# Performance work log

Hardware: AMD Instinct MI355X
Metric: run time of the kernel (lower is better)

## Reference

```python
import jax, jax.numpy as jnp
import numpy as np

N_HEADS = 16


def setup_inputs() -> dict:
    key = jax.random.key(0)
    ks = jax.random.split(key, 8)
    B, S, D = 4, 2048, 1024
    scale = 1.0 / np.sqrt(D)
    return {
        "x": jax.random.normal(ks[0], (B, S, D), dtype=jnp.float32),
        "Wq": jax.random.normal(ks[1], (D, D), dtype=jnp.float32) * scale,
        "bq": jax.random.normal(ks[2], (D,), dtype=jnp.float32) * 0.01,
        "Wk": jax.random.normal(ks[3], (D, D), dtype=jnp.float32) * scale,
        "bk": jax.random.normal(ks[4], (D,), dtype=jnp.float32) * 0.01,
        "Wv": jax.random.normal(ks[5], (D, D), dtype=jnp.float32) * scale,
        "bv": jax.random.normal(ks[6], (D,), dtype=jnp.float32) * 0.01,
        "mask": jax.random.randint(ks[7], (B, S), 0, 2, dtype=jnp.int32),
    }


def reference(x, Wq, bq, Wk, bk, Wv, bv, mask):
    B, S, D = x.shape
    H = N_HEADS
    W = D // H
    # QKV projections (Linear with weight stored input-major: y = x @ W + b)
    q = (x @ Wq + bq).reshape(B, S, H, W).transpose(0, 2, 1, 3)  # (B,H,S,W)
    k = (x @ Wk + bk).reshape(B, S, H, W).transpose(0, 2, 1, 3)
    v = (x @ Wv + bv).reshape(B, S, H, W).transpose(0, 2, 1, 3)
    # scaled dot-product scores: (B,H,S,S)
    scores = jnp.einsum("bhsw,bhtw->bhst", q, k) / jnp.sqrt(jnp.asarray(W, x.dtype))
    # mask==1 means masked (subtract large constant), per original code
    scores = scores - 10000.0 * mask[:, None, None, :].astype(x.dtype)
    attn = jax.nn.softmax(scores, axis=-1)  # dropout p=0 -> identity
    h = jnp.einsum("bhst,bhtw->bhsw", attn, v)  # (B,H,S,W)
    h = h.transpose(0, 2, 1, 3).reshape(B, S, D)
    return h
```

## Files before the change

kernel.cpp:

```cpp
#include <hip/hip_runtime.h>
#include <math.h>

#define B_NUM 4
#define S_LEN 2048
#define D_DIM 1024
#define H_NUM 16
#define W_DIM 64

typedef float4 f4;
typedef _Float16 f16;
typedef f16 f16x8 __attribute__((ext_vector_type(8)));
typedef f16 f16x4 __attribute__((ext_vector_type(4)));
typedef float floatx4 __attribute__((ext_vector_type(4)));

#define GLOAD_LDS16(gp, lp)                                                     \
    __builtin_amdgcn_global_load_lds(                                           \
        (const __attribute__((address_space(1))) void*)(gp),                    \
        (__attribute__((address_space(3))) void*)(lp), 16, 0, 0)

#define TR_BLOCKS   768
#define CAST_BLOCKS 8192

__global__ __launch_bounds__(256) void prep_kernel(
    const int* __restrict__ mask, short* __restrict__ fwdmap,
    int* __restrict__ cnt,
    const float* __restrict__ Wq, const float* __restrict__ Wk,
    const float* __restrict__ Wv, f16* __restrict__ wt16,
    const float* __restrict__ x, f16* __restrict__ x16)
{
    __shared__ __align__(16) char smraw[64 * 68 * 4];
    const int bx  = blockIdx.x;
    const int tid = threadIdx.x;

    if (bx < 4) {
        int* sc = (int*)smraw;
        const int b  = bx;
        const int t0 = tid * 8;
#pragma unroll
        for (int j = 0; j < 8; ++j) fwdmap[b * S_LEN + t0 + j] = 0;
        int kept[8], c = 0;
#pragma unroll
        for (int j = 0; j < 8; ++j) {
            kept[j] = (mask[b * S_LEN + t0 + j] == 0);
            c += kept[j];
        }
        sc[tid] = c;
        __syncthreads();
        for (int off = 1; off < 256; off <<= 1) {
            int add = (tid >= off) ? sc[tid - off] : 0;
            __syncthreads();
            sc[tid] += add;
            __syncthreads();
        }
        int base = sc[tid] - c;
#pragma unroll
        for (int j = 0; j < 8; ++j)
            if (kept[j]) fwdmap[b * S_LEN + (base++)] = (short)(t0 + j);
        if (tid == 255) {
            cnt[b * 4 + 0] = sc[255];
            cnt[b * 4 + 1] = (sc[255] + 63) & ~63;
            cnt[b * 4 + 2] = (sc[255] + 127) & ~127;
            cnt[b * 4 + 3] = (sc[255] + 255) & ~255;
        }
    } else if (bx < 4 + TR_BLOCKS) {
        float (*ts)[68] = (float(*)[68])smraw;
        const int idx = bx - 4;
        const int k0 = (idx & 15) * 64;
        const int n0 = ((idx >> 4) & 15) * 64;
        const int z  = idx >> 8;
        const float* Wsel = (z == 0) ? Wq : (z == 1) ? Wk : Wv;
        f16* outp = wt16 + (size_t)z * D_DIM * D_DIM;

        const int r  = tid >> 4;
        const int c4 = (tid & 15) * 4;
#pragma unroll
        for (int i = 0; i < 4; ++i) {
            f4 t = *(const f4*)&Wsel[(size_t)(k0 + r + i * 16) * D_DIM + n0 + c4];
            *(f4*)&ts[r + i * 16][c4] = t;
        }
        __syncthreads();
#pragma unroll
        for (int i = 0; i < 4; ++i) {
            int id2 = tid + i * 256;
            int nl = id2 >> 4;
            int k4 = (id2 & 15) * 4;
            f16x4 o;
#pragma unroll
            for (int j = 0; j < 4; ++j) o[j] = (f16)ts[k4 + j][nl];
            *(f16x4*)&outp[(size_t)(n0 + nl) * D_DIM + k0 + k4] = o;
        }
    } else {
        const size_t i = (size_t)(bx - 4 - TR_BLOCKS) * 256 + tid;
        f4 t = *(const f4*)&x[i * 4];
        f16x4 o;
        o[0] = (f16)t.x; o[1] = (f16)t.y; o[2] = (f16)t.z; o[3] = (f16)t.w;
        *(f16x4*)&x16[i * 4] = o;
    }
}

#define QSTAGE(BUF, K0) do {                                                    \
    _Pragma("unroll") for (int it_ = 0; it_ < 4; ++it_) {                       \
        int chunk_ = wid * 4 + it_;                                             \
        GLOAD_LDS16(&x16[(size_t)arows[it_] * D_DIM + (K0) + scw],              \
                    &As[BUF][chunk_ * 512]);                                    \
        GLOAD_LDS16(&Bg[(size_t)(chunk_ * 8 + srow) * D_DIM + (K0) + scw],      \
                    &Bs[BUF][chunk_ * 512]);                                    \
    } } while (0)

#define QCOMPUTE(BUF) do {                                                      \
    _Pragma("unroll") for (int kh_ = 0; kh_ < 2; ++kh_) {                       \
        const int csw_ = ((kh_ * 4 + quad) ^ (lx & 7)) * 8;                     \
        f16x8 af_[4], bf_[4];                                                   \
        _Pragma("unroll") for (int tm_ = 0; tm_ < 4; ++tm_)                     \
            af_[tm_] = *(const f16x8*)&As[BUF][(wm * 64 + tm_ * 16 + lx) * 64 + csw_]; \
        _Pragma("unroll") for (int tn_ = 0; tn_ < 4; ++tn_)                     \
            bf_[tn_] = *(const f16x8*)&Bs[BUF][(wn * 64 + tn_ * 16 + lx) * 64 + csw_]; \
        _Pragma("unroll") for (int tm_ = 0; tm_ < 4; ++tm_)                     \
        _Pragma("unroll") for (int tn_ = 0; tn_ < 4; ++tn_)                     \
            acc[tm_][tn_] = __builtin_amdgcn_mfma_f32_16x16x32_f16(             \
                af_[tm_], bf_[tn_], acc[tm_][tn_], 0, 0, 0);                    \
    } } while (0)

#define QVM0BAR() do {                                                          \
    asm volatile("s_waitcnt vmcnt(0)" ::: "memory");                            \
    __builtin_amdgcn_s_barrier();                                               \
    } while (0)

__global__ __launch_bounds__(256) void qkv_mfma_kernel(
    const f16* __restrict__ x16, const f16* __restrict__ wt16,
    const float* __restrict__ bq, const float* __restrict__ bk,
    const float* __restrict__ bv, const short* __restrict__ fwdmap,
    const int* __restrict__ cnt,
    f16* __restrict__ Qo, f16* __restrict__ Ko, f16* __restrict__ Vo)
{
    __shared__ f16 As[2][128 * 64];
    __shared__ f16 Bs[2][128 * 64];

    const int tid  = threadIdx.x;
    const int lane = tid & 63;
    const int wid  = tid >> 6;
    const int lx   = lane & 15;
    const int quad = lane >> 4;
    const int wm   = wid >> 1;
    const int wn   = wid & 1;

    const int r0    = blockIdx.y * 128;
    const int nt    = blockIdx.x;
    const int midx  = nt >> 3;
    const int c0    = (nt & 7) * 128;
    const int bB    = r0 >> 11;
    const int r0loc = r0 & (S_LEN - 1);

    if (midx > 0 && r0loc >= cnt[bB * 4 + 2]) return;

    const f16* Bg = wt16 + (size_t)midx * D_DIM * D_DIM + (size_t)c0 * D_DIM;

    const int srow = lane >> 3;
    const int scw  = ((lane & 7) ^ srow) * 8;

    int arows[4];
#pragma unroll
    for (int it = 0; it < 4; ++it) {
        int rl = (wid * 4 + it) * 8 + srow;
        arows[it] = (midx == 0)
            ? (r0 + rl)
            : (bB * S_LEN + (int)fwdmap[bB * S_LEN + r0loc + rl]);
    }

    floatx4 acc[4][4];
#pragma unroll
    for (int a = 0; a < 4; ++a)
#pragma unroll
        for (int b = 0; b < 4; ++b) { acc[a][b][0]=0.f; acc[a][b][1]=0.f; acc[a][b][2]=0.f; acc[a][b][3]=0.f; }

    QSTAGE(0, 0);
    QVM0BAR();

#pragma unroll 2
    for (int t = 0; t < 14; t += 2) {
        QSTAGE(1, (t + 1) * 64);
        QCOMPUTE(0);
        QVM0BAR();
        QSTAGE(0, (t + 2) * 64);
        QCOMPUTE(1);
        QVM0BAR();
    }
    QSTAGE(1, 15 * 64);
    QCOMPUTE(0);
    QVM0BAR();
    QCOMPUTE(1);

    const float* bp = (midx == 0) ? bq : (midx == 1) ? bk : bv;
    float bias[4];
#pragma unroll
    for (int tn = 0; tn < 4; ++tn)
        bias[tn] = bp[c0 + wn * 64 + tn * 16 + lx];

    if (midx == 0) {
#pragma unroll
        for (int tm = 0; tm < 4; ++tm) {
            int s = r0loc + wm * 64 + tm * 16 + quad * 4;
#pragma unroll
            for (int tn = 0; tn < 4; ++tn) {
                int gc = c0 + wn * 64 + tn * 16 + lx;
                int h = gc >> 6, w = gc & 63;
                size_t base = (((size_t)(bB * H_NUM + h)) * S_LEN + s) * W_DIM + w;
#pragma unroll
                for (int rr = 0; rr < 4; ++rr)
                    Qo[base + (size_t)rr * W_DIM] =
                        (f16)((acc[tm][tn][rr] + bias[tn]) * 0.125f);
            }
        }
    } else if (midx == 1) {
#pragma unroll
        for (int tm = 0; tm < 4; ++tm) {
            int jc = r0loc + wm * 64 + tm * 16 + quad * 4;
#pragma unroll
            for (int tn = 0; tn < 4; ++tn) {
                int gc = c0 + wn * 64 + tn * 16 + lx;
                int h = gc >> 6, w = gc & 63;
                size_t base = (((size_t)(bB * H_NUM + h)) * S_LEN + jc) * W_DIM + w;
#pragma unroll
                for (int rr = 0; rr < 4; ++rr)
                    Ko[base + (size_t)rr * W_DIM] = (f16)(acc[tm][tn][rr] + bias[tn]);
            }
        }
    } else {
#pragma unroll
        for (int tm = 0; tm < 4; ++tm) {
            int jc = r0loc + wm * 64 + tm * 16 + quad * 4;
#pragma unroll
            for (int tn = 0; tn < 4; ++tn) {
                int gc = c0 + wn * 64 + tn * 16 + lx;
                int h = gc >> 6, w = gc & 63;
                f16x4 v;
#pragma unroll
                for (int rr = 0; rr < 4; ++rr) v[rr] = (f16)(acc[tm][tn][rr] + bias[tn]);
                *(f16x4*)&Vo[(((size_t)(bB * H_NUM + h)) * W_DIM + w) * S_LEN + jc] = v;
            }
        }
    }
}

#define ASTAGE(BUF, K0) do {                                                    \
    _Pragma("unroll") for (int it_ = 0; it_ < 2; ++it_) {                       \
        int idx_ = tid + it_ * 256;                                             \
        int row_ = idx_ >> 3, ci_ = idx_ & 7;                                   \
        int sc_  = (ci_ ^ (row_ & 7)) * 8;                                      \
        int key_ = ((row_ >> 5) << 5) | (((row_ >> 2) & 3) << 3)                \
                 | (((row_ >> 4) & 1) << 2) | (row_ & 3);                       \
        GLOAD_LDS16(&Kg[(size_t)((K0) + key_) * W_DIM + sc_],                   \
                    (f16*)Ks[BUF] + idx_ * 8);                                  \
        GLOAD_LDS16(&Vg[(size_t)row_ * S_LEN + (K0) + sc_],                     \
                    (f16*)Vs[BUF] + idx_ * 8);                                  \
    } } while (0)

#define ACOMPUTE(BUF, K0) do {                                                  \
    const bool tail_ = ((K0) + 64 > count);                                     \
    f16x8 pb8[2][2];                                                            \
    _Pragma("unroll") for (int n = 0; n < 4; ++n) {                             \
        f16x8 ka0 = *(const f16x8*)&Ks[BUF][n * 16 + lx][((0 + quad) ^ swz) * 8]; \
        f16x8 ka1 = *(const f16x8*)&Ks[BUF][n * 16 + lx][((4 + quad) ^ swz) * 8]; \
        const int kb = (K0) + ((n >> 1) << 5) + (quad << 3) + ((n & 1) << 2);   \
        _Pragma("unroll") for (int u = 0; u < 2; ++u) {                         \
            floatx4 s; s[0]=0.f; s[1]=0.f; s[2]=0.f; s[3]=0.f;                  \
            s = __builtin_amdgcn_mfma_f32_16x16x32_f16(ka0, qb[u][0], s, 0, 0, 0); \
            s = __builtin_amdgcn_mfma_f32_16x16x32_f16(ka1, qb[u][1], s, 0, 0, 0); \
            float p[4], ls = 0.f;                                               \
            if (tail_) {                                                        \
                _Pragma("unroll") for (int r = 0; r < 4; ++r) {                 \
                    float sv = (kb + r < count) ? s[r] : -1.0e4f;               \
                    p[r] = __expf(sv); ls += p[r];                              \
                }                                                               \
            } else {                                                            \
                _Pragma("unroll") for (int r = 0; r < 4; ++r) {                 \
                    p[r] = __expf(s[r]); ls += p[r]; }                          \
            }                                                                   \
            lsum[u] += ls;                                                      \
            _Pragma("unroll") for (int r = 0; r < 4; ++r)                       \
                pb8[u][n >> 1][(n & 1) * 4 + r] = (f16)p[r];                    \
        }                                                                       \
    }                                                                           \
    _Pragma("unroll") for (int wb = 0; wb < 4; ++wb) {                          \
        _Pragma("unroll") for (int m = 0; m < 2; ++m) {                         \
            f16x8 va = *(const f16x8*)&Vs[BUF][wb * 16 + lx][((m * 4 + quad) ^ swz) * 8]; \
            _Pragma("unroll") for (int u = 0; u < 2; ++u)                       \
                o[u][wb] = __builtin_amdgcn_mfma_f32_16x16x32_f16(              \
                    va, pb8[u][m], o[u][wb], 0, 0, 0);                          \
        }                                                                       \
    } } while (0)

__global__ __launch_bounds__(256) void attn_kernel(
    const f16* __restrict__ Q, const f16* __restrict__ Kc,
    const f16* __restrict__ Vct, const int* __restrict__ cnt,
    float* __restrict__ out)
{
    __shared__ f16 Ks[2][64][64];
    __shared__ f16 Vs[2][64][64];

    const int tid  = threadIdx.x;
    const int lane = tid & 63;
    const int wid  = tid >> 6;
    const int lx   = lane & 15;
    const int quad = lane >> 4;
    const int qt = blockIdx.x, h = blockIdx.y, bb = blockIdx.z;

    const int count = cnt[bb * 4 + 0];
    const int scp   = cnt[bb * 4 + 1];
    const int ntile = scp >> 6;

    const size_t hoff = ((size_t)(bb * H_NUM + h)) * S_LEN * W_DIM;
    const f16* Qg = Q + hoff + (size_t)qt * 128 * W_DIM;
    const f16* Kg = Kc + hoff;
    const f16* Vg = Vct + hoff;

    f16x8 qb[2][2];
#pragma unroll
    for (int u = 0; u < 2; ++u) {
        int qrow = u * 64 + wid * 16 + lx;
        qb[u][0] = *(const f16x8*)&Qg[(size_t)qrow * W_DIM + quad * 8];
        qb[u][1] = *(const f16x8*)&Qg[(size_t)qrow * W_DIM + 32 + quad * 8];
    }

    floatx4 o[2][4];
    float lsum[2] = {0.f, 0.f};
#pragma unroll
    for (int u = 0; u < 2; ++u)
#pragma unroll
        for (int wb = 0; wb < 4; ++wb) { o[u][wb][0]=0.f; o[u][wb][1]=0.f; o[u][wb][2]=0.f; o[u][wb][3]=0.f; }

    const int swz = lx & 7;

    ASTAGE(0, 0);
    asm volatile("s_waitcnt vmcnt(0)" ::: "memory");
    __builtin_amdgcn_s_barrier();

    for (int t = 0; t < ntile; t += 2) {
        if (t + 1 < ntile) ASTAGE(1, (t + 1) * 64);
        ACOMPUTE(0, t * 64);
        asm volatile("s_waitcnt vmcnt(0)" ::: "memory");
        __builtin_amdgcn_s_barrier();
        if (t + 1 < ntile) {
            if (t + 2 < ntile) ASTAGE(0, (t + 2) * 64);
            ACOMPUTE(1, (t + 1) * 64);
            asm volatile("s_waitcnt vmcnt(0)" ::: "memory");
            __builtin_amdgcn_s_barrier();
        }
    }

#pragma unroll
    for (int u = 0; u < 2; ++u) {
        float ls = lsum[u];
        ls += __shfl_xor(ls, 16);
        ls += __shfl_xor(ls, 32);
        const float rl = 1.0f / ls;
        const int q = qt * 128 + u * 64 + wid * 16 + lx;
        const size_t base = ((size_t)bb * S_LEN + q) * D_DIM + h * W_DIM;
#pragma unroll
        for (int wb = 0; wb < 4; ++wb) {
            f4 r;
            r.x = o[u][wb][0] * rl;
            r.y = o[u][wb][1] * rl;
            r.z = o[u][wb][2] * rl;
            r.w = o[u][wb][3] * rl;
            *(f4*)&out[base + wb * 16 + quad * 4] = r;
        }
    }
}

extern "C" void kernel_launch(void* const* d_in, const int* in_sizes, int n_in,
                              void* d_out, int out_size, void* d_ws, size_t ws_size,
                              hipStream_t stream)
{
    const float* x    = (const float*)d_in[0];
    const float* Wq   = (const float*)d_in[1];
    const float* bq   = (const float*)d_in[2];
    const float* Wk   = (const float*)d_in[3];
    const float* bk   = (const float*)d_in[4];
    const float* Wv   = (const float*)d_in[5];
    const float* bv   = (const float*)d_in[6];
    const int*   mask = (const int*)d_in[7];
    float* out = (float*)d_out;

    const size_t per = (size_t)B_NUM * H_NUM * S_LEN * W_DIM;
    f16*   Q      = (f16*)d_ws;
    f16*   Kc     = Q + per;
    f16*   Vct    = Kc + per;
    f16*   x16    = Vct + per;
    f16*   wt16   = x16 + (size_t)(B_NUM * S_LEN) * D_DIM;
    int*   cnt    = (int*)(wt16 + (size_t)3 * D_DIM * D_DIM);
    short* fwdmap = (short*)(cnt + 4 * B_NUM);

    prep_kernel<<<4 + TR_BLOCKS + CAST_BLOCKS, 256, 0, stream>>>(
        mask, fwdmap, cnt, Wq, Wk, Wv, wt16, x, x16);
    qkv_mfma_kernel<<<dim3(24, 64), 256, 0, stream>>>(
        x16, wt16, bq, bk, bv, fwdmap, cnt, Q, Kc, Vct);
    attn_kernel<<<dim3(S_LEN / 128, H_NUM, B_NUM), 256, 0, stream>>>(
        Q, Kc, Vct, cnt, out);
}
```

Before: 218.7 us.

## Use exp2 with folded log2e scale, packed f16 conversion, and MFMA row sums

Folds log2(e) into the Q scaling so the softmax exponent becomes a native exp2 instead of __expf. It converts probabilities with packed round-toward-zero f16 conversion instead of per-element casts. The row sum is now accumulated by an extra MFMA against a ones vector, using the same f16-rounded probabilities, instead of scalar adds and shuffles. The aim is to cut VALU work in the softmax inner loop, at the cost of four extra MFMAs per tile and slightly different rounding.

```diff
diff --git a/kernel.cpp b/kernel.cpp
--- a/kernel.cpp
+++ b/kernel.cpp
@@ -12,6 +12,15 @@
 typedef f16 f16x8 __attribute__((ext_vector_type(8)));
 typedef f16 f16x4 __attribute__((ext_vector_type(4)));
 typedef float floatx4 __attribute__((ext_vector_type(4)));
+typedef unsigned int u32;
+typedef u32 u32x4 __attribute__((ext_vector_type(4)));
+
+#if __has_builtin(__builtin_amdgcn_exp2f)
+#define FEXP2(x) __builtin_amdgcn_exp2f(x)
+#else
+#define FEXP2(x) __expf((x) * 0.6931471805599453f)
+#endif
+#define QSCALE 0.18033688011f
 
 #define GLOAD_LDS16(gp, lp)                                                     \
     __builtin_amdgcn_global_load_lds(                                           \
@@ -208,7 +217,7 @@
 #pragma unroll
                 for (int rr = 0; rr < 4; ++rr)
                     Qo[base + (size_t)rr * W_DIM] =
-                        (f16)((acc[tm][tn][rr] + bias[tn]) * 0.125f);
+                        (f16)((acc[tm][tn][rr] + bias[tn]) * QSCALE);
             }
         }
     } else if (midx == 1) {
@@ -257,7 +266,7 @@
 
 #define ACOMPUTE(BUF, K0) do {                                                  \
     const bool tail_ = ((K0) + 64 > count);                                     \
-    f16x8 pb8[2][2];                                                            \
+    u32x4 pbu[2][2];                                                            \
     _Pragma("unroll") for (int n = 0; n < 4; ++n) {                             \
         f16x8 ka0 = *(const f16x8*)&Ks[BUF][n * 16 + lx][((0 + quad) ^ swz) * 8]; \
         f16x8 ka1 = *(const f16x8*)&Ks[BUF][n * 16 + lx][((4 + quad) ^ swz) * 8]; \
@@ -266,19 +275,18 @@
             floatx4 s; s[0]=0.f; s[1]=0.f; s[2]=0.f; s[3]=0.f;                  \
             s = __builtin_amdgcn_mfma_f32_16x16x32_f16(ka0, qb[u][0], s, 0, 0, 0); \
             s = __builtin_amdgcn_mfma_f32_16x16x32_f16(ka1, qb[u][1], s, 0, 0, 0); \
-            float p[4], ls = 0.f;                                               \
+            float p[4];                                                         \
             if (tail_) {                                                        \
-                _Pragma("unroll") for (int r = 0; r < 4; ++r) {                 \
-                    float sv = (kb + r < count) ? s[r] : -1.0e4f;               \
-                    p[r] = __expf(sv); ls += p[r];                              \
-                }                                                               \
+                _Pragma("unroll") for (int r = 0; r < 4; ++r)                   \
+                    p[r] = FEXP2((kb + r < count) ? s[r] : -1.0e4f);            \
             } else {                                                            \
-                _Pragma("unroll") for (int r = 0; r < 4; ++r) {                 \
-                    p[r] = __expf(s[r]); ls += p[r]; }                          \
+                _Pragma("unroll") for (int r = 0; r < 4; ++r)                   \
+                    p[r] = FEXP2(s[r]);                                         \
             }                                                                   \
-            lsum[u] += ls;                                                      \
-            _Pragma("unroll") for (int r = 0; r < 4; ++r)                       \
-                pb8[u][n >> 1][(n & 1) * 4 + r] = (f16)p[r];                    \
+            auto t0_ = __builtin_amdgcn_cvt_pkrtz(p[0], p[1]);                  \
+            auto t1_ = __builtin_amdgcn_cvt_pkrtz(p[2], p[3]);                  \
+            pbu[u][n >> 1][(n & 1) * 2 + 0] = __builtin_bit_cast(u32, t0_);     \
+            pbu[u][n >> 1][(n & 1) * 2 + 1] = __builtin_bit_cast(u32, t1_);     \
         }                                                                       \
     }                                                                           \
     _Pragma("unroll") for (int wb = 0; wb < 4; ++wb) {                          \
@@ -286,9 +294,14 @@
             f16x8 va = *(const f16x8*)&Vs[BUF][wb * 16 + lx][((m * 4 + quad) ^ swz) * 8]; \
             _Pragma("unroll") for (int u = 0; u < 2; ++u)                       \
                 o[u][wb] = __builtin_amdgcn_mfma_f32_16x16x32_f16(              \
-                    va, pb8[u][m], o[u][wb], 0, 0, 0);                          \
+                    va, __builtin_bit_cast(f16x8, pbu[u][m]), o[u][wb], 0, 0, 0); \
         }                                                                       \
-    } } while (0)
+    }                                                                           \
+    _Pragma("unroll") for (int m = 0; m < 2; ++m)                               \
+        _Pragma("unroll") for (int u = 0; u < 2; ++u)                           \
+            o1[u] = __builtin_amdgcn_mfma_f32_16x16x32_f16(                     \
+                ones8, __builtin_bit_cast(f16x8, pbu[u][m]), o1[u], 0, 0, 0);   \
+    } while (0)
 
 __global__ __launch_bounds__(256) void attn_kernel(
     const f16* __restrict__ Q, const f16* __restrict__ Kc,
@@ -322,12 +335,17 @@
         qb[u][1] = *(const f16x8*)&Qg[(size_t)qrow * W_DIM + 32 + quad * 8];
     }
 
+    const f16x8 ones8 = {(f16)1.f, (f16)1.f, (f16)1.f, (f16)1.f,
+                         (f16)1.f, (f16)1.f, (f16)1.f, (f16)1.f};
+
     floatx4 o[2][4];
-    float lsum[2] = {0.f, 0.f};
-#pragma unroll
-    for (int u = 0; u < 2; ++u)
+    floatx4 o1[2];
+#pragma unroll
+    for (int u = 0; u < 2; ++u) {
+        o1[u][0]=0.f; o1[u][1]=0.f; o1[u][2]=0.f; o1[u][3]=0.f;
 #pragma unroll
         for (int wb = 0; wb < 4; ++wb) { o[u][wb][0]=0.f; o[u][wb][1]=0.f; o[u][wb][2]=0.f; o[u][wb][3]=0.f; }
+    }
 
     const int swz = lx & 7;
 
@@ -350,10 +368,7 @@
 
 #pragma unroll
     for (int u = 0; u < 2; ++u) {
-        float ls = lsum[u];
-        ls += __shfl_xor(ls, 16);
-        ls += __shfl_xor(ls, 32);
-        const float rl = 1.0f / ls;
+        const float rl = 1.0f / o1[u][0];
         const int q = qt * 128 + u * 64 + wid * 16 + lx;
         const size_t base = ((size_t)bb * S_LEN + q) * D_DIM + h * W_DIM;
 #pragma unroll
```

Measured after the change: 215.8 us, median of 2. No clear change (-1.3%).
